# Optimization experiments

Hardware: AMD Instinct MI355X
Metric: run time of the kernel (lower is better)

Reference implementation:

```python
import jax, jax.numpy as jnp
import numpy as np

WS = 7          # window size
NUM_HEADS = 8


def _depthwise_conv3x3(x, w, b):
    # x: [B, C, H, W], w: [C, 1, 3, 3], groups=C depthwise, padding=1
    y = jax.lax.conv_general_dilated(
        x, w, window_strides=(1, 1), padding='SAME',
        dimension_numbers=('NCHW', 'OIHW', 'NCHW'),
        feature_group_count=x.shape[1])
    return y + b[None, :, None, None]


def setup_inputs() -> dict:
    key = jax.random.key(0)
    k1, k2, k3 = jax.random.split(key, 3)
    B, H, W, C = 8, 112, 112, 256
    qkv = jax.random.normal(k1, (3, B, H * W, C), dtype=jnp.float32)
    lepe_w = jax.random.normal(k2, (C, 1, 3, 3), dtype=jnp.float32) * 0.1
    lepe_b = jax.random.normal(k3, (C,), dtype=jnp.float32) * 0.1
    return {"qkv": qkv, "lepe_w": lepe_w, "lepe_b": lepe_b, "H": H, "W": W}


def reference(qkv, lepe_w, lepe_b, H, W):
    q, k, v = qkv[0], qkv[1], qkv[2]          # each [B, N, C]
    B, N, C = v.shape
    hd = C // NUM_HEADS
    scale = hd ** -0.5
    Gh, Gw = H // WS, W // WS                 # H, W assumed divisible by WS

    # LePE: depthwise 3x3 conv on v viewed as image
    lepe = _depthwise_conv3x3(v.transpose(0, 2, 1).reshape(B, C, H, W), lepe_w, lepe_b)
    lepe = lepe.reshape(B, C, N).transpose(0, 2, 1)   # [B, N, C]

    def to_windows(x):
        # [B, N, C] -> [B*Gh*Gw, heads, ws*ws, hd]
        x = x.reshape(B, Gh, WS, Gw, WS, NUM_HEADS, hd)
        return x.transpose(0, 1, 3, 5, 2, 4, 6).reshape(B * Gh * Gw, NUM_HEADS, WS * WS, hd)

    qg = to_windows(q) * scale
    kg = to_windows(k)
    vg = to_windows(v)

    attn = jax.nn.softmax(jnp.einsum('ghnd,ghmd->ghnm', qg, kg), axis=-1)
    out = jnp.einsum('ghnm,ghmd->ghnd', attn, vg)     # [BG, heads, n, hd]

    # group2image: inverse window partition -> [B, N, C]
    out = out.reshape(B, Gh, Gw, NUM_HEADS, WS, WS, hd)
    out = out.transpose(0, 1, 4, 2, 5, 3, 6).reshape(B, N, C)
    return out + lepe
```

## Files before the change

### kernel.cpp

```cpp
#include <hip/hip_runtime.h>

#define WS   7
#define NH   8
#define HD   32
#define WIN  49
#define HALO 9
#define VHST 36
#define LST  34

typedef __fp16 h2  __attribute__((ext_vector_type(2)));
typedef __fp16 v4h __attribute__((ext_vector_type(4)));
typedef float  v4f __attribute__((ext_vector_type(4)));

__global__ __launch_bounds__(64)
void win_attn_lepe(const float* __restrict__ qkv,
                   const float* __restrict__ lw,
                   const float* __restrict__ lb,
                   float* __restrict__ out,
                   int B, int H, int W, int C)
{
    const int N  = H * W;
    const int Gw = W / WS;
    const int G  = (H / WS) * Gw;

    const int unit = blockIdx.x;
    const int wid  = unit >> 3;
    const int h    = unit & 7;
    const int b    = wid / G;
    const int g    = wid % G;
    const int gy   = g / Gw, gx = g % Gw;
    const int row0 = gy * WS, col0 = gx * WS;
    const int c0   = h * HD;

    const size_t plane = (size_t)B * N * C;
    const float* qb = qkv + (size_t)b * N * C;
    const float* kb = qb + plane;
    const float* vb = qb + 2 * plane;

    const int l  = threadIdx.x;
    const int lr = l & 15;
    const int gq = l >> 4;

    __shared__ __fp16 sVh  [HALO * HALO * VHST];
    __shared__ __fp16 sW2  [16 * 20];
    __shared__ __fp16 sLepe[WIN * LST];

    for (int idx = l; idx < HALO * HALO * 8; idx += 64) {
        int p  = idx >> 3;
        int d4 = (idx & 7) * 4;
        int ry = row0 - 1 + p / HALO, rx = col0 - 1 + p % HALO;
        bool in = (ry >= 0 && ry < H && rx >= 0 && rx < W);
        float4 f = make_float4(0.f, 0.f, 0.f, 0.f);
        if (in) f = *reinterpret_cast<const float4*>(vb + ((size_t)ry * W + rx) * C + c0 + d4);
        h2 a  = __builtin_amdgcn_cvt_pkrtz(f.x, f.y);
        h2 b2 = __builtin_amdgcn_cvt_pkrtz(f.z, f.w);
        v4h v4 = { a.x, a.y, b2.x, b2.y };
        *reinterpret_cast<v4h*>(&sVh[p * VHST + d4]) = v4;
    }
    for (int i = l; i < 288; i += 64) {
        int d = i / 9, t = i - d * 9;
        sW2[(d >> 1) * 20 + 2 * t + (d & 1)] = (__fp16)lw[(size_t)(c0 + d) * 9 + t];
    }
    __syncthreads();

    const float bias0 = lb[c0 + lr];
    const float bias1 = lb[c0 + 16 + lr];

    auto pixoff = [&](int p) -> size_t {
        p = p > 48 ? 48 : p;
        int r = row0 + p / WS, c = col0 + p % WS;
        return ((size_t)r * W + c) * C + c0;
    };

    const float scale = 0.17677669529663687f;

    v4h qf[4][2];
    #pragma unroll
    for (int m = 0; m < 4; ++m) {
        size_t off = pixoff(16 * m + lr);
        #pragma unroll
        for (int s = 0; s < 2; ++s) {
            float4 f = *reinterpret_cast<const float4*>(qb + off + 16 * s + 4 * gq);
            h2 a  = __builtin_amdgcn_cvt_pkrtz(f.x * scale, f.y * scale);
            h2 b2 = __builtin_amdgcn_cvt_pkrtz(f.z * scale, f.w * scale);
            qf[m][s] = v4h{ a.x, a.y, b2.x, b2.y };
        }
    }
    v4h kf[4][2];
    #pragma unroll
    for (int t = 0; t < 4; ++t) {
        size_t off = pixoff(16 * t + lr);
        #pragma unroll
        for (int s = 0; s < 2; ++s) {
            float4 f = *reinterpret_cast<const float4*>(kb + off + 16 * s + 4 * gq);
            h2 a  = __builtin_amdgcn_cvt_pkrtz(f.x, f.y);
            h2 b2 = __builtin_amdgcn_cvt_pkrtz(f.z, f.w);
            kf[t][s] = v4h{ a.x, a.y, b2.x, b2.y };
        }
    }

    v4h vf[4][2];
    #pragma unroll
    for (int s4 = 0; s4 < 4; ++s4) {
        #pragma unroll
        for (int j = 0; j < 4; ++j) {
            int p  = 16 * s4 + 4 * gq + j;
            int pc = p > 48 ? 48 : p;
            int hp = (pc / WS + 1) * HALO + pc % WS + 1;
            int base = hp * VHST + lr;
            vf[s4][0][j] = sVh[base];
            vf[s4][1][j] = sVh[base + 16];
        }
    }

    {
        h2 w2r[9];
        #pragma unroll
        for (int t = 0; t < 9; ++t)
            w2r[t] = *reinterpret_cast<const h2*>(&sW2[lr * 20 + 2 * t]);
        #pragma unroll 1
        for (int it = 0; it < 13; ++it) {
            int pix = it * 4 + gq;
            if (pix < WIN) {
                int wy = pix / WS, wx = pix - (pix / WS) * WS;
                h2 acc = h2{ (__fp16)0.f, (__fp16)0.f };
                #pragma unroll
                for (int dh = 0; dh < 3; ++dh)
                    #pragma unroll
                    for (int dw = 0; dw < 3; ++dw) {
                        h2 v = *reinterpret_cast<const h2*>(
                            &sVh[((wy + dh) * HALO + (wx + dw)) * VHST + 2 * lr]);
                        acc += w2r[dh * 3 + dw] * v;
                    }
                *reinterpret_cast<h2*>(&sLepe[pix * LST + 2 * lr]) = acc;
            }
        }
    }
    __syncthreads();

    #pragma unroll 1
    for (int mq = 0; mq < 4; ++mq) {
        v4f sa[4] = { v4f{0,0,0,0}, v4f{0,0,0,0}, v4f{0,0,0,0}, v4f{0,0,0,0} };
        #pragma unroll
        for (int tk = 0; tk < 4; ++tk)
            #pragma unroll
            for (int s = 0; s < 2; ++s)
                sa[tk] = __builtin_amdgcn_mfma_f32_16x16x16f16(kf[tk][s], qf[mq][s], sa[tk], 0, 0, 0);

        float den = 0.f;
        #pragma unroll
        for (int tk = 0; tk < 4; ++tk)
            #pragma unroll
            for (int r = 0; r < 4; ++r) {
                float e = (16 * tk + 4 * gq + r < WIN) ? __expf(sa[tk][r] - 3.f) : 0.f;
                sa[tk][r] = e;
                den += e;
            }
        den += __shfl_xor(den, 16);
        den += __shfl_xor(den, 32);
        const float inv = __builtin_amdgcn_rcpf(den);

        v4f oa0 = v4f{0,0,0,0}, oa1 = v4f{0,0,0,0};
        #pragma unroll
        for (int s4 = 0; s4 < 4; ++s4) {
            h2 p01 = __builtin_amdgcn_cvt_pkrtz(sa[s4][0] * inv, sa[s4][1] * inv);
            h2 p23 = __builtin_amdgcn_cvt_pkrtz(sa[s4][2] * inv, sa[s4][3] * inv);
            v4h pa = v4h{ p01.x, p01.y, p23.x, p23.y };
            oa0 = __builtin_amdgcn_mfma_f32_16x16x16f16(pa, vf[s4][0], oa0, 0, 0, 0);
            oa1 = __builtin_amdgcn_mfma_f32_16x16x16f16(pa, vf[s4][1], oa1, 0, 0, 0);
        }

        #pragma unroll
        for (int r = 0; r < 4; ++r) {
            int p = 16 * mq + 4 * gq + r;
            if (p < WIN) {
                int rr = row0 + p / WS, cc = col0 + p % WS;
                float* dst = out + ((size_t)b * N + (size_t)rr * W + cc) * C + c0 + lr;
                dst[0]  = oa0[r] + (float)sLepe[p * LST + lr]      + bias0;
                dst[16] = oa1[r] + (float)sLepe[p * LST + 16 + lr] + bias1;
            }
        }
    }
}

extern "C" void kernel_launch(void* const* d_in, const int* in_sizes, int n_in,
                              void* d_out, int out_size, void* d_ws, size_t ws_size,
                              hipStream_t stream) {
    const float* qkv = (const float*)d_in[0];
    const float* lw  = (const float*)d_in[1];
    const float* lb  = (const float*)d_in[2];
    float* out = (float*)d_out;

    const int H = 112, W = 112;
    const int C = in_sizes[2];
    const int N = H * W;
    const int B = in_sizes[0] / (3 * N * C);
    const int G = (H / WS) * (W / WS);

    const int units = B * G * NH;
    win_attn_lepe<<<units, 64, 0, stream>>>(qkv, lw, lb, out, B, H, W, C);
}
```

Before: 145.8 us.

## Pack four independent window-head units per block with wave-local LDS fences and exp2 softmax

Each block now runs four waves, each handling its own window-head unit with private LDS slices, so the 64-thread blocks become 256-thread blocks and each __syncthreads is replaced by a wave-local lgkmcnt wait. The softmax folds log2(e) into the query scale, uses the raw v_exp_f32 instruction, and skips the exponentials of the padded key tile using the known 49-key layout. This targets per-block launch and scheduling overhead and cuts exp work, but it relies on units dividing evenly by four and changes the constant shift used in the exponent.

```diff
diff --git a/kernel.cpp b/kernel.cpp
--- a/kernel.cpp
+++ b/kernel.cpp
@@ -7,12 +7,21 @@
 #define HALO 9
 #define VHST 36
 #define LST  34
+#define UPB  4
 
 typedef __fp16 h2  __attribute__((ext_vector_type(2)));
 typedef __fp16 v4h __attribute__((ext_vector_type(4)));
 typedef float  v4f __attribute__((ext_vector_type(4)));
 
-__global__ __launch_bounds__(64)
+#define WAVE_LDS_FENCE() asm volatile("s_waitcnt lgkmcnt(0)" ::: "memory")
+
+__device__ __forceinline__ float fexp2(float x) {
+    float r;
+    asm("v_exp_f32 %0, %1" : "=v"(r) : "v"(x));
+    return r;
+}
+
+__global__ __launch_bounds__(64 * UPB, 4)
 void win_attn_lepe(const float* __restrict__ qkv,
                    const float* __restrict__ lw,
                    const float* __restrict__ lb,
@@ -23,7 +32,10 @@
     const int Gw = W / WS;
     const int G  = (H / WS) * Gw;
 
-    const int unit = blockIdx.x;
+    const int wave = threadIdx.x >> 6;
+    const int l    = threadIdx.x & 63;
+
+    const int unit = blockIdx.x * UPB + wave;
     const int wid  = unit >> 3;
     const int h    = unit & 7;
     const int b    = wid / G;
@@ -37,13 +49,12 @@
     const float* kb = qb + plane;
     const float* vb = qb + 2 * plane;
 
-    const int l  = threadIdx.x;
     const int lr = l & 15;
     const int gq = l >> 4;
 
-    __shared__ __fp16 sVh  [HALO * HALO * VHST];
-    __shared__ __fp16 sW2  [16 * 20];
-    __shared__ __fp16 sLepe[WIN * LST];
+    __shared__ __fp16 sVh  [UPB][HALO * HALO * VHST];
+    __shared__ __fp16 sW2  [UPB][16 * 20];
+    __shared__ __fp16 sLepe[UPB][WIN * LST];
 
     for (int idx = l; idx < HALO * HALO * 8; idx += 64) {
         int p  = idx >> 3;
@@ -55,13 +66,13 @@
         h2 a  = __builtin_amdgcn_cvt_pkrtz(f.x, f.y);
         h2 b2 = __builtin_amdgcn_cvt_pkrtz(f.z, f.w);
         v4h v4 = { a.x, a.y, b2.x, b2.y };
-        *reinterpret_cast<v4h*>(&sVh[p * VHST + d4]) = v4;
+        *reinterpret_cast<v4h*>(&sVh[wave][p * VHST + d4]) = v4;
     }
     for (int i = l; i < 288; i += 64) {
         int d = i / 9, t = i - d * 9;
-        sW2[(d >> 1) * 20 + 2 * t + (d & 1)] = (__fp16)lw[(size_t)(c0 + d) * 9 + t];
-    }
-    __syncthreads();
+        sW2[wave][(d >> 1) * 20 + 2 * t + (d & 1)] = (__fp16)lw[(size_t)(c0 + d) * 9 + t];
+    }
+    WAVE_LDS_FENCE();
 
     const float bias0 = lb[c0 + lr];
     const float bias1 = lb[c0 + 16 + lr];
@@ -72,7 +83,8 @@
         return ((size_t)r * W + c) * C + c0;
     };
 
-    const float scale = 0.17677669529663687f;
+    const float scale = 0.17677669529663687f * 1.4426950408889634f;
+    const float ESHIFT = 4.328085122666891f;
 
     v4h qf[4][2];
     #pragma unroll
@@ -108,8 +120,8 @@
             int pc = p > 48 ? 48 : p;
             int hp = (pc / WS + 1) * HALO + pc % WS + 1;
             int base = hp * VHST + lr;
-            vf[s4][0][j] = sVh[base];
-            vf[s4][1][j] = sVh[base + 16];
+            vf[s4][0][j] = sVh[wave][base];
+            vf[s4][1][j] = sVh[wave][base + 16];
         }
     }
 
@@ -117,7 +129,7 @@
         h2 w2r[9];
         #pragma unroll
         for (int t = 0; t < 9; ++t)
-            w2r[t] = *reinterpret_cast<const h2*>(&sW2[lr * 20 + 2 * t]);
+            w2r[t] = *reinterpret_cast<const h2*>(&sW2[wave][lr * 20 + 2 * t]);
         #pragma unroll 1
         for (int it = 0; it < 13; ++it) {
             int pix = it * 4 + gq;
@@ -129,14 +141,14 @@
                     #pragma unroll
                     for (int dw = 0; dw < 3; ++dw) {
                         h2 v = *reinterpret_cast<const h2*>(
-                            &sVh[((wy + dh) * HALO + (wx + dw)) * VHST + 2 * lr]);
+                            &sVh[wave][((wy + dh) * HALO + (wx + dw)) * VHST + 2 * lr]);
                         acc += w2r[dh * 3 + dw] * v;
                     }
-                *reinterpret_cast<h2*>(&sLepe[pix * LST + 2 * lr]) = acc;
+                *reinterpret_cast<h2*>(&sLepe[wave][pix * LST + 2 * lr]) = acc;
             }
         }
     }
-    __syncthreads();
+    WAVE_LDS_FENCE();
 
     #pragma unroll 1
     for (int mq = 0; mq < 4; ++mq) {
@@ -149,13 +161,18 @@
 
         float den = 0.f;
         #pragma unroll
-        for (int tk = 0; tk < 4; ++tk)
+        for (int tk = 0; tk < 3; ++tk)
             #pragma unroll
             for (int r = 0; r < 4; ++r) {
-                float e = (16 * tk + 4 * gq + r < WIN) ? __expf(sa[tk][r] - 3.f) : 0.f;
+                float e = fexp2(sa[tk][r] - ESHIFT);
                 sa[tk][r] = e;
                 den += e;
             }
+        {
+            float e0 = (gq == 0) ? fexp2(sa[3][0] - ESHIFT) : 0.f;
+            sa[3][0] = e0; sa[3][1] = 0.f; sa[3][2] = 0.f; sa[3][3] = 0.f;
+            den += e0;
+        }
         den += __shfl_xor(den, 16);
         den += __shfl_xor(den, 32);
         const float inv = __builtin_amdgcn_rcpf(den);
@@ -176,8 +193,8 @@
             if (p < WIN) {
                 int rr = row0 + p / WS, cc = col0 + p % WS;
                 float* dst = out + ((size_t)b * N + (size_t)rr * W + cc) * C + c0 + lr;
-                dst[0]  = oa0[r] + (float)sLepe[p * LST + lr]      + bias0;
-                dst[16] = oa1[r] + (float)sLepe[p * LST + 16 + lr] + bias1;
+                dst[0]  = oa0[r] + (float)sLepe[wave][p * LST + lr]      + bias0;
+                dst[16] = oa1[r] + (float)sLepe[wave][p * LST + 16 + lr] + bias1;
             }
         }
     }
@@ -198,5 +215,5 @@
     const int G = (H / WS) * (W / WS);
 
     const int units = B * G * NH;
-    win_attn_lepe<<<units, 64, 0, stream>>>(qkv, lw, lb, out, B, H, W, C);
+    win_attn_lepe<<<units / UPB, 64 * UPB, 0, stream>>>(qkv, lw, lb, out, B, H, W, C);
 }
```

Result: faster. 126.4 us, median of 2 (-13.3%).
